# Optimization experiments

Measured on AMD Instinct MI355X. Metric: run time of the kernel, lower is better.

Reference implementation:

```python
import jax, jax.numpy as jnp
import numpy as np

N = 65536      # n query/support points
NN = 34        # neighbors per point
K = 15         # kernel points
IN_F = 64
OUT_F = 64
RADIUS = 2.5
KP_EXTENT_CFG = 1.0
DENSITY = 5.0
EXTENT = KP_EXTENT_CFG * RADIUS / DENSITY  # effective KP_extent = 0.5
BN_EPS = 1e-6
LRELU_SLOPE = 0.1
POINT_DIM = 4  # modulated=True -> 3 offset dims + 1 modulation per kernel point


def make_kernel_points():
    # Deterministic stand-in for the precomputed kernel dispositions loaded
    # from disk in KPConv (fixed='center': first point at origin). Points lie
    # inside a ball of radius 1.5 * extent.
    rng = np.random.RandomState(42)
    kp = rng.normal(size=(K, 3))
    kp /= np.linalg.norm(kp, axis=1, keepdims=True)
    kp *= rng.uniform(0.3, 1.0, size=(K, 1))
    kp[0] = 0.0
    return jnp.asarray(kp * (1.5 * EXTENT), dtype=jnp.float32)


def setup_inputs() -> dict:
    key = jax.random.key(0)
    ks = jax.random.split(key, 8)
    query_points = jax.random.uniform(ks[0], (N, 3), dtype=jnp.float32)
    support_points = jax.random.uniform(ks[1], (N, 3), dtype=jnp.float32)
    neighbors_indices = jax.random.randint(ks[2], (N, NN), 0, N, dtype=jnp.int32)
    features = jax.random.normal(ks[3], (N, IN_F), dtype=jnp.float32)
    # weight_variable: truncated normal with std sqrt(2/size[-1])
    weight = jax.random.truncated_normal(ks[4], -2.0, 2.0, (K, IN_F, OUT_F), jnp.float32) * np.sqrt(2.0 / OUT_F)
    off_dim = POINT_DIM * K
    offset_weight = jax.random.truncated_normal(ks[5], -2.0, 2.0, (K, IN_F, off_dim), jnp.float32) * np.sqrt(2.0 / off_dim)
    offset_bias = jnp.zeros((off_dim,), jnp.float32)
    bn_gamma = jnp.ones((OUT_F,), jnp.float32)
    bn_beta = jnp.zeros((OUT_F,), jnp.float32)
    kernel_points = make_kernel_points()
    return dict(query_points=query_points, support_points=support_points,
                neighbors_indices=neighbors_indices, features=features,
                weight=weight, offset_weight=offset_weight, offset_bias=offset_bias,
                bn_gamma=bn_gamma, bn_beta=bn_beta, kernel_points=kernel_points)


def _influence(sq_dist):
    # KP_influence='linear': relu(1 - d / extent)
    return jax.nn.relu(1.0 - jnp.sqrt(sq_dist) / EXTENT)


def reference(query_points, support_points, neighbors_indices, features,
              weight, offset_weight, offset_bias, bn_gamma, bn_beta, kernel_points):
    n = query_points.shape[0]
    # Shadow point (far away) / shadow feature (zeros) appended at index n0
    supp_pad = jnp.concatenate([support_points, jnp.full((1, 3), 1e6, jnp.float32)], 0)
    feat_pad = jnp.concatenate([features, jnp.zeros((1, IN_F), jnp.float32)], 0)

    neigh_pts = supp_pad[neighbors_indices] - query_points[:, None, :]   # [n,nn,3]
    neigh_feats = feat_pad[neighbors_indices]                            # [n,nn,in]

    # ---- rigid KPConv producing per-point offsets (+ modulations) ----
    sq0 = jnp.sum((neigh_pts[:, :, None, :] - kernel_points[None, None]) ** 2, -1)  # [n,nn,K]
    w0 = _influence(sq0)
    wf0 = jnp.einsum('nak,nac->nkc', w0, neigh_feats)                    # [n,K,in]
    f0 = jnp.einsum('nkc,kcd->nd', wf0, offset_weight) + offset_bias     # [n,4K]
    offsets = f0[:, :3 * K].reshape(n, K, 3) * EXTENT                    # rescale to layer extent
    modulations = 2.0 * jax.nn.sigmoid(f0[:, 3 * K:])                    # [n,K]

    # ---- deformable KPConv ----
    def_kp = kernel_points[None] + offsets                               # [n,K,3]
    sq = jnp.sum((neigh_pts[:, :, None, :] - def_kp[:, None, :, :]) ** 2, -1)  # [n,nn,K]
    w = _influence(sq)                                                   # aggregation_mode='sum'
    wf = jnp.einsum('nak,nac->nkc', w, neigh_feats) * modulations[:, :, None]
    x = jnp.einsum('nkc,kco->no', wf, weight)                            # [n,out]

    # BatchNorm1d (training-mode batch stats, eps=1e-6) + LeakyReLU(0.1)
    mean = x.mean(0)
    var = x.var(0)
    x = (x - mean) * jax.lax.rsqrt(var + BN_EPS) * bn_gamma + bn_beta
    return jnp.where(x >= 0, x, LRELU_SLOPE * x)
```

## Files before the change

kernel.cpp:

```cpp
#include <hip/hip_runtime.h>
#include <math.h>

#define NPTS 65536

using half8   = __attribute__((ext_vector_type(8))) _Float16;
using half4   = __attribute__((ext_vector_type(4))) _Float16;
using floatx4 = __attribute__((ext_vector_type(4))) float;

__global__ __launch_bounds__(256) void k_prep(
    const float* __restrict__ ow, const float* __restrict__ w,
    const float* __restrict__ feat,
    _Float16* __restrict__ owt, _Float16* __restrict__ wt,
    _Float16* __restrict__ featH)
{
  int b = blockIdx.x;
  if (b < 256) {
    int i = b * 256 + threadIdx.x;
    int d = i >> 10, kc = i & 1023, c = kc >> 4, k = kc & 15;
    owt[i] = (k < 15 && d < 60) ? (_Float16)ow[(k * 64 + c) * 60 + d] : (_Float16)0.f;
    wt[i]  = (k < 15) ? (_Float16)w[(k * 64 + c) * 64 + d] : (_Float16)0.f;
  } else {
    int j = (b - 256) * 256 + threadIdx.x;
    float4 f = ((const float4*)feat)[j];
    half4 h = {(_Float16)f.x, (_Float16)f.y, (_Float16)f.z, (_Float16)f.w};
    ((half4*)featH)[j] = h;
  }
}

__global__ __launch_bounds__(256, 3) void k_fused(
    const float* __restrict__ query, const float* __restrict__ support,
    const int* __restrict__ nidx, const _Float16* __restrict__ featH,
    const float* __restrict__ kpts, const float* __restrict__ obias,
    const _Float16* __restrict__ owt, const _Float16* __restrict__ wt,
    float* __restrict__ outx)
{
  __shared__ float                  npx[16][34], npy[16][34], npz[16][34];
  __shared__ unsigned short         sidx[16][34];
  __shared__ __align__(16) _Float16 fT[4][64 * 32];
  __shared__ unsigned int           fx2[4][64];
  __shared__ __align__(16) _Float16 wfh[16 * 520];
  __shared__ float                  dk[16][64];

  const int tid  = threadIdx.x;
  const int wave = tid >> 6, lane = tid & 63;
  const int quad = lane >> 4, mm = lane & 15;
  const int base = blockIdx.x * 16;
  _Float16* fTw = fT[wave];
  unsigned int* fTw32 = (unsigned int*)fTw;
  unsigned int* fx2w = fx2[wave];
  const floatx4 fz = {0.f, 0.f, 0.f, 0.f};
  const int me = (mm < 15) ? mm : 14;

  for (int s = tid; s < 544; s += 256) {
    int pt = s / 34, a = s - pt * 34;
    int n = base + pt;
    int id = nidx[n * 34 + a];
    npx[pt][a] = support[id * 3 + 0] - query[n * 3 + 0];
    npy[pt][a] = support[id * 3 + 1] - query[n * 3 + 1];
    npz[pt][a] = support[id * 3 + 2] - query[n * 3 + 2];
    sidx[pt][a] = (unsigned short)id;
  }
  __syncthreads();

  auto load_g = [&](int pl, uint4* g0, uint4* g1) {
    #pragma unroll
    for (int it = 0; it < 3; ++it) {
      int task = it * 64 + lane;
      if (task < 136) {
        int rp = task >> 3, ch = task & 7;
        int i0 = (int)sidx[pl][2 * rp], i1 = (int)sidx[pl][2 * rp + 1];
        g0[it] = *(const uint4*)(featH + i0 * 64 + ch * 8);
        g1[it] = *(const uint4*)(featH + i1 * 64 + ch * 8);
      }
    }
  };
  auto transpose_g = [&](const uint4* g0, const uint4* g1) {
    #pragma unroll
    for (int it = 0; it < 3; ++it) {
      int task = it * 64 + lane;
      if (task < 136) {
        int rp = task >> 3, ch = task & 7;
        const uint* p0 = (const uint*)&g0[it];
        const uint* p1 = (const uint*)&g1[it];
        if (rp < 16) {
          int chunk = rp >> 2, o = rp & 3;
          #pragma unroll
          for (int cc = 0; cc < 8; ++cc) {
            int c  = ch * 8 + cc;
            int pc = chunk ^ ((ch ^ cc) & 3);
            uint v = __builtin_amdgcn_perm(p1[cc >> 1], p0[cc >> 1],
                                           (cc & 1) ? 0x07060302u : 0x05040100u);
            fTw32[c * 16 + pc * 4 + o] = v;
          }
        } else {
          #pragma unroll
          for (int cc = 0; cc < 8; ++cc) {
            uint v = __builtin_amdgcn_perm(p1[cc >> 1], p0[cc >> 1],
                                           (cc & 1) ? 0x07060302u : 0x05040100u);
            fx2w[ch * 8 + cc] = v;
          }
        }
      }
    }
  };

  auto conv_point = [&](int pl, float kx, float ky, float kz, const float* md,
                        floatx4* hold) {
    half8 a0;
    #pragma unroll
    for (int j = 0; j < 8; ++j) {
      int a = quad * 8 + j;
      float dx = npx[pl][a] - kx, dy = npy[pl][a] - ky, dz = npz[pl][a] - kz;
      float wv = 1.f - 2.f * sqrtf(dx * dx + dy * dy + dz * dz);
      a0[j] = (_Float16)fmaxf(wv, 0.f);
    }
    float w32, w33;
    {
      float dx = npx[pl][32] - kx, dy = npy[pl][32] - ky, dz = npz[pl][32] - kz;
      w32 = fmaxf(1.f - 2.f * sqrtf(dx * dx + dy * dy + dz * dz), 0.f);
      dx = npx[pl][33] - kx; dy = npy[pl][33] - ky; dz = npz[pl][33] - kz;
      w33 = fmaxf(1.f - 2.f * sqrtf(dx * dx + dy * dy + dz * dz), 0.f);
    }
    float w32r[4], w33r[4];
    #pragma unroll
    for (int r = 0; r < 4; ++r) {
      int src = (quad * 4 + r) << 2;
      w32r[r] = __int_as_float(__builtin_amdgcn_ds_bpermute(src, __float_as_int(w32)));
      w33r[r] = __int_as_float(__builtin_amdgcn_ds_bpermute(src, __float_as_int(w33)));
    }

    floatx4 acc[4];
    #pragma unroll
    for (int ct = 0; ct < 4; ++ct) {
      int c  = ct * 16 + mm;
      int pc = quad ^ (((c >> 3) ^ c) & 3);
      half8 b = *(const half8*)(fTw + c * 32 + pc * 8);
      acc[ct] = __builtin_amdgcn_mfma_f32_16x16x32_f16(a0, b, fz, 0, 0, 0);
    }
    #pragma unroll
    for (int ct = 0; ct < 4; ++ct) {
      int c = ct * 16 + mm;
      uint fp = fx2w[c];
      _Float16 lo = __builtin_bit_cast(_Float16, (unsigned short)(fp & 0xffffu));
      _Float16 hi = __builtin_bit_cast(_Float16, (unsigned short)(fp >> 16));
      float flo = (float)lo, fhi = (float)hi;
      #pragma unroll
      for (int r = 0; r < 4; ++r)
        acc[ct][r] = (acc[ct][r] + w32r[r] * flo + w33r[r] * fhi) * md[r];
    }

    _Float16* wp = wfh + pl * 520;
    #pragma unroll
    for (int ct = 0; ct < 2; ++ct) {
      half4 h = {(_Float16)acc[ct][0], (_Float16)acc[ct][1],
                 (_Float16)acc[ct][2], (_Float16)acc[ct][3]};
      *(half4*)(wp + (ct * 16 + mm) * 16 + quad * 4) = h;
    }
    hold[0] = acc[2]; hold[1] = acc[3];
  };

  auto write_hold = [&](const floatx4 (*hold)[2]) {
    #pragma unroll
    for (int pp = 0; pp < 4; ++pp) {
      _Float16* wp = wfh + (wave * 4 + pp) * 520;
      #pragma unroll
      for (int ct = 0; ct < 2; ++ct) {
        const floatx4& a = hold[pp][ct];
        half4 h = {(_Float16)a[0], (_Float16)a[1], (_Float16)a[2], (_Float16)a[3]};
        *(half4*)(wp + (ct * 16 + mm) * 16 + quad * 4) = h;
      }
    }
  };

  auto gemm_half = [&](const _Float16* bmat, int koff, floatx4& A, floatx4& B) {
    const _Float16* brow = bmat + (wave * 16 + mm) * 1024 + koff;
    const _Float16* arow = wfh + mm * 520;
    #pragma unroll
    for (int k2 = 0; k2 < 16; ++k2) {
      half8 af = *(const half8*)(arow + k2 * 32 + quad * 8);
      half8 bf = *(const half8*)(brow + k2 * 32 + quad * 8);
      if (k2 & 1) B = __builtin_amdgcn_mfma_f32_16x16x32_f16(af, bf, B, 0, 0, 0);
      else        A = __builtin_amdgcn_mfma_f32_16x16x32_f16(af, bf, A, 0, 0, 0);
    }
  };

  uint4 G0[2][3], G1[2][3];
  floatx4 hold[4][2];
  const float one4[4] = {1.f, 1.f, 1.f, 1.f};

  {
    float k0x = kpts[me * 3 + 0], k0y = kpts[me * 3 + 1], k0z = kpts[me * 3 + 2];
    load_g(wave * 4, G0[0], G1[0]);
    #pragma unroll
    for (int pp = 0; pp < 4; ++pp) {
      int pl = wave * 4 + pp;
      if (pp < 3) load_g(pl + 1, G0[(pp + 1) & 1], G1[(pp + 1) & 1]);
      transpose_g(G0[pp & 1], G1[pp & 1]);
      conv_point(pl, k0x, k0y, k0z, one4, hold[pp]);
    }
  }
  load_g(wave * 4, G0[0], G1[0]);
  __syncthreads();

  {
    floatx4 A = fz, B = fz;
    gemm_half(owt, 0, A, B);
    __syncthreads();
    write_hold(hold);
    __syncthreads();
    gemm_half(owt, 512, A, B);
    int d = wave * 16 + mm;
    float bv = (d < 60) ? obias[d] : 0.f;
    float kv = (d < 45) ? kpts[d] : 0.f;
    #pragma unroll
    for (int r = 0; r < 4; ++r) {
      int pt = quad * 4 + r;
      float v = A[r] + B[r] + bv;
      float o = (d < 45) ? (kv + 0.5f * v)
                         : (2.f / (1.f + expf(-v)));
      dk[pt][d] = o;
    }
  }
  __syncthreads();

  #pragma unroll
  for (int pp = 0; pp < 4; ++pp) {
    int pl = wave * 4 + pp;
    if (pp < 3) load_g(pl + 1, G0[(pp + 1) & 1], G1[(pp + 1) & 1]);
    float kx = dk[pl][me * 3 + 0], ky = dk[pl][me * 3 + 1], kz = dk[pl][me * 3 + 2];
    float md[4];
    #pragma unroll
    for (int r = 0; r < 4; ++r) {
      int k = quad * 4 + r;
      md[r] = (k < 15) ? dk[pl][45 + k] : 1.f;
    }
    transpose_g(G0[pp & 1], G1[pp & 1]);
    conv_point(pl, kx, ky, kz, md, hold[pp]);
  }
  __syncthreads();

  {
    floatx4 A = fz, B = fz;
    gemm_half(wt, 0, A, B);
    __syncthreads();
    write_hold(hold);
    __syncthreads();
    gemm_half(wt, 512, A, B);
    int d = wave * 16 + mm;
    #pragma unroll
    for (int r = 0; r < 4; ++r)
      outx[(base + quad * 4 + r) * 64 + d] = A[r] + B[r];
  }
}

__global__ __launch_bounds__(256) void k_stats(
    const float* __restrict__ x, float* __restrict__ stats)
{
  __shared__ float red[512];
  const int tid = threadIdx.x;
  const int c = tid & 63, g = tid >> 6;
  float s1 = 0.f, s2 = 0.f;
  for (int r = blockIdx.x * 4 + g; r < NPTS; r += 1024) {
    float v = x[r * 64 + c];
    s1 += v; s2 += v * v;
  }
  red[tid] = s1; red[256 + tid] = s2;
  __syncthreads();
  if (tid < 64) {
    s1 = red[tid] + red[tid + 64] + red[tid + 128] + red[tid + 192];
    s2 = red[256 + tid] + red[256 + tid + 64] + red[256 + tid + 128] + red[256 + tid + 192];
    atomicAdd(&stats[c], s1);
    atomicAdd(&stats[64 + c], s2);
  }
}

__global__ __launch_bounds__(256) void k_norm(
    float* __restrict__ x, const float* __restrict__ stats,
    const float* __restrict__ gamma, const float* __restrict__ beta)
{
  const int i = blockIdx.x * 256 + threadIdx.x;
  float4 v = ((float4*)x)[i];
  const int c0 = (i * 4) & 63;
  float o[4] = {v.x, v.y, v.z, v.w};
  #pragma unroll
  for (int j = 0; j < 4; ++j) {
    int c = c0 + j;
    float mean = stats[c] * (1.f / NPTS);
    float var  = stats[64 + c] * (1.f / NPTS) - mean * mean;
    float s = rsqrtf(var + 1e-6f) * gamma[c];
    float y = (o[j] - mean) * s + beta[c];
    o[j] = (y >= 0.f) ? y : 0.1f * y;
  }
  float4 rv = {o[0], o[1], o[2], o[3]};
  ((float4*)x)[i] = rv;
}

extern "C" void kernel_launch(void* const* d_in, const int* in_sizes, int n_in,
                              void* d_out, int out_size, void* d_ws, size_t ws_size,
                              hipStream_t stream)
{
  const float* query   = (const float*)d_in[0];
  const float* support = (const float*)d_in[1];
  const int*   nidx    = (const int*)d_in[2];
  const float* feat    = (const float*)d_in[3];
  const float* weight  = (const float*)d_in[4];
  const float* oweight = (const float*)d_in[5];
  const float* obias   = (const float*)d_in[6];
  const float* gamma   = (const float*)d_in[7];
  const float* beta    = (const float*)d_in[8];
  const float* kpts    = (const float*)d_in[9];
  float* x = (float*)d_out;

  char* ws = (char*)d_ws;
  _Float16* featH = (_Float16*)ws;
  _Float16* owt   = (_Float16*)(ws + 8388608);
  _Float16* wt    = (_Float16*)(ws + 8519680);
  float*    stats = (float*)(ws + 8650752);

  hipMemsetAsync(stats, 0, 512, stream);
  k_prep<<<4352, 256, 0, stream>>>(oweight, weight, feat, owt, wt, featH);
  k_fused<<<4096, 256, 0, stream>>>(query, support, nidx, featH, kpts, obias,
                                    owt, wt, x);
  k_stats<<<256, 256, 0, stream>>>(x, stats);
  k_norm<<<4096, 256, 0, stream>>>(x, stats, gamma, beta);
}
```

Baseline: 309.5 us.

## Compute influence weights in packed fp16, raise occupancy, replace stats atomics with two-pass reduce

Neighbor coordinates and deformed kernel points are now kept in fp16 shared memory, and the influence weights are computed with packed half2 arithmetic. This cuts LDS footprint and VALU work and allows four resident blocks per CU instead of three. The transposed feature tile gets an extra row swizzle to reduce bank conflicts. The BN statistics pass now writes per-block partials that a separate reduce kernel sums, replacing the atomics and the memset. Doing the distance math in fp16 costs accuracy in the influence weights and the offsets, and the extra launch adds fixed overhead.

Result: slower. 403.8 us (+30.5%).

```diff
diff --git a/kernel.cpp b/kernel.cpp
--- a/kernel.cpp
+++ b/kernel.cpp
@@ -5,6 +5,7 @@
 
 using half8   = __attribute__((ext_vector_type(8))) _Float16;
 using half4   = __attribute__((ext_vector_type(4))) _Float16;
+using half2v  = __attribute__((ext_vector_type(2))) _Float16;
 using floatx4 = __attribute__((ext_vector_type(4))) float;
 
 __global__ __launch_bounds__(256) void k_prep(
@@ -27,19 +28,19 @@
   }
 }
 
-__global__ __launch_bounds__(256, 3) void k_fused(
+__global__ __launch_bounds__(256, 4) void k_fused(
     const float* __restrict__ query, const float* __restrict__ support,
     const int* __restrict__ nidx, const _Float16* __restrict__ featH,
     const float* __restrict__ kpts, const float* __restrict__ obias,
     const _Float16* __restrict__ owt, const _Float16* __restrict__ wt,
     float* __restrict__ outx)
 {
-  __shared__ float                  npx[16][34], npy[16][34], npz[16][34];
+  __shared__ _Float16               nph[3][16][34];
   __shared__ unsigned short         sidx[16][34];
-  __shared__ __align__(16) _Float16 fT[4][64 * 32];
+  __shared__ __align__(16) _Float16 fT[4][2048];
   __shared__ unsigned int           fx2[4][64];
   __shared__ __align__(16) _Float16 wfh[16 * 520];
-  __shared__ float                  dk[16][64];
+  __shared__ _Float16               dkh[16][64];
 
   const int tid  = threadIdx.x;
   const int wave = tid >> 6, lane = tid & 63;
@@ -55,9 +56,9 @@
     int pt = s / 34, a = s - pt * 34;
     int n = base + pt;
     int id = nidx[n * 34 + a];
-    npx[pt][a] = support[id * 3 + 0] - query[n * 3 + 0];
-    npy[pt][a] = support[id * 3 + 1] - query[n * 3 + 1];
-    npz[pt][a] = support[id * 3 + 2] - query[n * 3 + 2];
+    nph[0][pt][a] = (_Float16)(support[id * 3 + 0] - query[n * 3 + 0]);
+    nph[1][pt][a] = (_Float16)(support[id * 3 + 1] - query[n * 3 + 1]);
+    nph[2][pt][a] = (_Float16)(support[id * 3 + 2] - query[n * 3 + 2]);
     sidx[pt][a] = (unsigned short)id;
   }
   __syncthreads();
@@ -88,9 +89,10 @@
           for (int cc = 0; cc < 8; ++cc) {
             int c  = ch * 8 + cc;
             int pc = chunk ^ ((ch ^ cc) & 3);
+            int rr = c ^ (ch & 1);
             uint v = __builtin_amdgcn_perm(p1[cc >> 1], p0[cc >> 1],
                                            (cc & 1) ? 0x07060302u : 0x05040100u);
-            fTw32[c * 16 + pc * 4 + o] = v;
+            fTw32[rr * 16 + pc * 4 + o] = v;
           }
         } else {
           #pragma unroll
@@ -104,22 +106,36 @@
     }
   };
 
-  auto conv_point = [&](int pl, float kx, float ky, float kz, const float* md,
-                        floatx4* hold) {
+  auto infl_pair = [&](int pl, int pj, half2v kx2, half2v ky2, half2v kz2,
+                       _Float16& w0, _Float16& w1) {
+    const half2v* px = (const half2v*)&nph[0][pl][0];
+    const half2v* py = (const half2v*)&nph[1][pl][0];
+    const half2v* pz = (const half2v*)&nph[2][pl][0];
+    half2v dx = px[pj] - kx2, dy = py[pj] - ky2, dz = pz[pj] - kz2;
+    half2v dd = dx * dx + dy * dy + dz * dz;
+    _Float16 s0 = __builtin_sqrtf16(dd.x);
+    _Float16 s1 = __builtin_sqrtf16(dd.y);
+    _Float16 v0 = (_Float16)1.f - (_Float16)2.f * s0;
+    _Float16 v1 = (_Float16)1.f - (_Float16)2.f * s1;
+    w0 = (v0 > (_Float16)0.f) ? v0 : (_Float16)0.f;
+    w1 = (v1 > (_Float16)0.f) ? v1 : (_Float16)0.f;
+  };
+
+  auto conv_point = [&](int pl, _Float16 kxh, _Float16 kyh, _Float16 kzh,
+                        const float* md, floatx4* hold) {
+    half2v kx2 = {kxh, kxh}, ky2 = {kyh, kyh}, kz2 = {kzh, kzh};
     half8 a0;
     #pragma unroll
-    for (int j = 0; j < 8; ++j) {
-      int a = quad * 8 + j;
-      float dx = npx[pl][a] - kx, dy = npy[pl][a] - ky, dz = npz[pl][a] - kz;
-      float wv = 1.f - 2.f * sqrtf(dx * dx + dy * dy + dz * dz);
-      a0[j] = (_Float16)fmaxf(wv, 0.f);
+    for (int t = 0; t < 4; ++t) {
+      _Float16 w0, w1;
+      infl_pair(pl, quad * 4 + t, kx2, ky2, kz2, w0, w1);
+      a0[2 * t] = w0; a0[2 * t + 1] = w1;
     }
     float w32, w33;
     {
-      float dx = npx[pl][32] - kx, dy = npy[pl][32] - ky, dz = npz[pl][32] - kz;
-      w32 = fmaxf(1.f - 2.f * sqrtf(dx * dx + dy * dy + dz * dz), 0.f);
-      dx = npx[pl][33] - kx; dy = npy[pl][33] - ky; dz = npz[pl][33] - kz;
-      w33 = fmaxf(1.f - 2.f * sqrtf(dx * dx + dy * dy + dz * dz), 0.f);
+      _Float16 w0, w1;
+      infl_pair(pl, 16, kx2, ky2, kz2, w0, w1);
+      w32 = (float)w0; w33 = (float)w1;
     }
     float w32r[4], w33r[4];
     #pragma unroll
@@ -133,8 +149,9 @@
     #pragma unroll
     for (int ct = 0; ct < 4; ++ct) {
       int c  = ct * 16 + mm;
+      int rr = c ^ ((c >> 3) & 1);
       int pc = quad ^ (((c >> 3) ^ c) & 3);
-      half8 b = *(const half8*)(fTw + c * 32 + pc * 8);
+      half8 b = *(const half8*)(fTw + rr * 32 + pc * 8);
       acc[ct] = __builtin_amdgcn_mfma_f32_16x16x32_f16(a0, b, fz, 0, 0, 0);
     }
     #pragma unroll
@@ -189,7 +206,9 @@
   const float one4[4] = {1.f, 1.f, 1.f, 1.f};
 
   {
-    float k0x = kpts[me * 3 + 0], k0y = kpts[me * 3 + 1], k0z = kpts[me * 3 + 2];
+    _Float16 k0x = (_Float16)kpts[me * 3 + 0];
+    _Float16 k0y = (_Float16)kpts[me * 3 + 1];
+    _Float16 k0z = (_Float16)kpts[me * 3 + 2];
     load_g(wave * 4, G0[0], G1[0]);
     #pragma unroll
     for (int pp = 0; pp < 4; ++pp) {
@@ -218,7 +237,7 @@
       float v = A[r] + B[r] + bv;
       float o = (d < 45) ? (kv + 0.5f * v)
                          : (2.f / (1.f + expf(-v)));
-      dk[pt][d] = o;
+      dkh[pt][d] = (_Float16)o;
     }
   }
   __syncthreads();
@@ -227,12 +246,14 @@
   for (int pp = 0; pp < 4; ++pp) {
     int pl = wave * 4 + pp;
     if (pp < 3) load_g(pl + 1, G0[(pp + 1) & 1], G1[(pp + 1) & 1]);
-    float kx = dk[pl][me * 3 + 0], ky = dk[pl][me * 3 + 1], kz = dk[pl][me * 3 + 2];
+    _Float16 kx = dkh[pl][me * 3 + 0];
+    _Float16 ky = dkh[pl][me * 3 + 1];
+    _Float16 kz = dkh[pl][me * 3 + 2];
     float md[4];
     #pragma unroll
     for (int r = 0; r < 4; ++r) {
       int k = quad * 4 + r;
-      md[r] = (k < 15) ? dk[pl][45 + k] : 1.f;
+      md[r] = (k < 15) ? (float)dkh[pl][45 + k] : 1.f;
     }
     transpose_g(G0[pp & 1], G1[pp & 1]);
     conv_point(pl, kx, ky, kz, md, hold[pp]);
@@ -254,13 +275,13 @@
 }
 
 __global__ __launch_bounds__(256) void k_stats(
-    const float* __restrict__ x, float* __restrict__ stats)
+    const float* __restrict__ x, float* __restrict__ part)
 {
   __shared__ float red[512];
   const int tid = threadIdx.x;
   const int c = tid & 63, g = tid >> 6;
   float s1 = 0.f, s2 = 0.f;
-  for (int r = blockIdx.x * 4 + g; r < NPTS; r += 1024) {
+  for (int r = blockIdx.x * 4 + g; r < NPTS; r += 512) {
     float v = x[r * 64 + c];
     s1 += v; s2 += v * v;
   }
@@ -269,9 +290,23 @@
   if (tid < 64) {
     s1 = red[tid] + red[tid + 64] + red[tid + 128] + red[tid + 192];
     s2 = red[256 + tid] + red[256 + tid + 64] + red[256 + tid + 128] + red[256 + tid + 192];
-    atomicAdd(&stats[c], s1);
-    atomicAdd(&stats[64 + c], s2);
-  }
+    part[blockIdx.x * 128 + c] = s1;
+    part[blockIdx.x * 128 + 64 + c] = s2;
+  }
+}
+
+__global__ __launch_bounds__(256) void k_reduce(
+    const float* __restrict__ part, float* __restrict__ stats)
+{
+  __shared__ float red[256];
+  const int tid = threadIdx.x;
+  const int c = tid & 127, half = tid >> 7;
+  float s = 0.f;
+  #pragma unroll 4
+  for (int b = half * 64; b < half * 64 + 64; ++b) s += part[b * 128 + c];
+  red[tid] = s;
+  __syncthreads();
+  if (tid < 128) stats[tid] = red[tid] + red[tid + 128];
 }
 
 __global__ __launch_bounds__(256) void k_norm(
@@ -315,12 +350,13 @@
   _Float16* featH = (_Float16*)ws;
   _Float16* owt   = (_Float16*)(ws + 8388608);
   _Float16* wt    = (_Float16*)(ws + 8519680);
-  float*    stats = (float*)(ws + 8650752);
-
-  hipMemsetAsync(stats, 0, 512, stream);
+  float*    part  = (float*)(ws + 8650752);
+  float*    stats = (float*)(ws + 8716288);
+
   k_prep<<<4352, 256, 0, stream>>>(oweight, weight, feat, owt, wt, featH);
   k_fused<<<4096, 256, 0, stream>>>(query, support, nidx, featH, kpts, obias,
                                     owt, wt, x);
-  k_stats<<<256, 256, 0, stream>>>(x, stats);
+  k_stats<<<128, 256, 0, stream>>>(x, part);
+  k_reduce<<<1, 256, 0, stream>>>(part, stats);
   k_norm<<<4096, 256, 0, stream>>>(x, stats, gamma, beta);
 }
```
